# Optimization experiments

Hardware: AMD Instinct MI355X
Metric: run time of the kernel (lower is better)

## Reference

```python
import jax, jax.numpy as jnp
import numpy as np

N_NODES = 100000
N_EDGES = 1600000
D = 64


def _leaky(x, slope=0.2):
    return jnp.where(x >= 0, x, slope * x)


def setup_inputs() -> dict:
    key = jax.random.key(0)
    ks = jax.random.split(key, 13)
    x = jax.random.normal(ks[0], (N_NODES, D), dtype=jnp.float32)
    edge_index = jax.random.randint(ks[1], (2, N_EDGES), 0, N_NODES, dtype=jnp.int64)
    e_hat = jax.random.normal(ks[2], (N_EDGES, D), dtype=jnp.float32)
    s = 1.0 / np.sqrt(D)
    def lin(kw, kb):
        W = jax.random.uniform(kw, (D, D), dtype=jnp.float32, minval=-s, maxval=s)
        b = jax.random.uniform(kb, (D,), dtype=jnp.float32, minval=-s, maxval=s)
        return W, b
    U_w, U_b = lin(ks[3], ks[4])
    V_w, V_b = lin(ks[5], ks[6])
    A_w, A_b = lin(ks[7], ks[8])
    B_w, B_b = lin(ks[9], ks[10])
    C_w, C_b = lin(ks[11], ks[12])
    return {"x": x, "e_hat": e_hat, "edge_index": edge_index,
            "U_w": U_w, "U_b": U_b, "V_w": V_w, "V_b": V_b,
            "A_w": A_w, "A_b": A_b, "B_w": B_w, "B_b": B_b,
            "C_w": C_w, "C_b": C_b}


def reference(x, e_hat, edge_index, U_w, U_b, V_w, V_b, A_w, A_b, B_w, B_b, C_w, C_b):
    n = x.shape[0]
    src = edge_index[0]  # [E]
    dst = edge_index[1]  # [E]

    x_i = x[src]  # [E, D] (pre-update x, as in original)
    x_j = x[dst]  # [E, D]

    # scatter_softmax of e_hat over segments keyed by src, per feature column
    m = jax.ops.segment_max(e_hat, src, num_segments=n)        # [N, D]
    ex = jnp.exp(e_hat - m[src])                               # [E, D]
    denom = jax.ops.segment_sum(ex, src, num_segments=n)      # [N, D]
    e = ex / denom[src]                                        # [E, D]

    # gated aggregation: scatter_add(V(x_j) * e)
    y = (x_j @ V_w.T + V_b) * e                                # [E, D]
    y = jax.ops.segment_sum(y, src, num_segments=n)            # [N, D]

    x_new = x + _leaky(x @ U_w.T + U_b + y)
    e_new = e_hat + _leaky(x_i @ A_w.T + A_b + x_j @ B_w.T + B_b + e_hat @ C_w.T + C_b)
    return x_new, e_new
```

## Files before the change

### kernel.cpp

```cpp
#include <hip/hip_runtime.h>
#include <math.h>
#include <stdint.h>

typedef __attribute__((ext_vector_type(8))) short bf16x8;
typedef __attribute__((ext_vector_type(4))) float f32x4;

static __device__ __forceinline__ float leaky(float v) {
    return v >= 0.f ? v : 0.2f * v;
}

static __device__ __forceinline__ short f2bf(float f) {
    uint32_t u = __float_as_uint(f);
    u = (u + 0x7FFFu + ((u >> 16) & 1u)) >> 16;
    return (short)u;
}

static __device__ __forceinline__ float b2f(unsigned short us) {
    return __uint_as_float(((uint32_t)us) << 16);
}

static __device__ __forceinline__ bf16x8 pack8(float4 a, float4 b) {
    bf16x8 r;
    r[0] = f2bf(a.x); r[1] = f2bf(a.y); r[2] = f2bf(a.z); r[3] = f2bf(a.w);
    r[4] = f2bf(b.x); r[5] = f2bf(b.y); r[6] = f2bf(b.z); r[7] = f2bf(b.w);
    return r;
}

static __device__ __forceinline__ void split2(int bid, int na, int nb,
                                              bool& second, int& idx) {
    int nm = na < nb ? na : nb;
    if (bid < 2 * nm) { idx = bid >> 1; second = (bid & 1) != 0; }
    else { int r = bid - 2 * nm; second = nb > na; idx = nm + r; }
}

static __device__ __forceinline__ void load_wfrags_f32(const float* __restrict__ W,
                                                       int lo, int hi, bf16x8 wf[4][2]) {
#pragma unroll
    for (int ct = 0; ct < 4; ++ct)
#pragma unroll
        for (int s = 0; s < 2; ++s) {
            const float* cp = W + (size_t)(ct * 16 + lo) * 64 + s * 32 + hi * 8;
            wf[ct][s] = pack8(*(const float4*)cp, *(const float4*)(cp + 4));
        }
}

static __device__ __forceinline__ void load_wfrags(const unsigned short* __restrict__ Wb,
                                                   int lo, int hi, bf16x8 wf[4][2]) {
#pragma unroll
    for (int ct = 0; ct < 4; ++ct)
#pragma unroll
        for (int s = 0; s < 2; ++s)
            wf[ct][s] = *(const bf16x8*)(Wb + (size_t)(ct * 16 + lo) * 64 + s * 32 + hi * 8);
}

__global__ __launch_bounds__(256) void pre_fused(
        const float* __restrict__ x,
        const float* __restrict__ Uw, const float* __restrict__ Ub,
        const float* __restrict__ Vw, const float* __restrict__ Vb,
        const float* __restrict__ Aw, const float* __restrict__ Ab,
        const float* __restrict__ Bw, const float* __restrict__ Bb,
        const float* __restrict__ Cw, unsigned short* __restrict__ Cbf,
        float* __restrict__ Ux, unsigned short* __restrict__ Vxb,
        unsigned short* __restrict__ Axb, unsigned short* __restrict__ Bxb, int n,
        const int* __restrict__ src, int* __restrict__ deg, int e,
        int gemmBlocks, int histBlocks)
{
    int t = threadIdx.x;
    int bid = blockIdx.x;

    if (bid >= gemmBlocks + histBlocks) {
        int i = (bid - gemmBlocks - histBlocks) * 256 + t;
        Cbf[i] = (unsigned short)f2bf(Cw[i]);
        return;
    }

    bool isHist; int half;
    split2(bid, gemmBlocks, histBlocks, isHist, half);

    if (isHist) {
        int i0 = half * 1024 + t * 4;
        if (i0 + 3 < e) {
            int4 s4 = *(const int4*)(src + i0);
            atomicAdd(&deg[s4.x], 1); atomicAdd(&deg[s4.y], 1);
            atomicAdd(&deg[s4.z], 1); atomicAdd(&deg[s4.w], 1);
        } else {
#pragma unroll
            for (int k = 0; k < 4; ++k) { int i = i0 + k; if (i < e) atomicAdd(&deg[src[i]], 1); }
        }
        return;
    }

    int w = t >> 6, l = t & 63;
    int lo = l & 15, hi = l >> 4;
    long base = (long)half * 64;

    const float* Wp = (w == 0) ? Uw : (w == 1) ? Vw : (w == 2) ? Aw : Bw;
    const float* bp = (w == 0) ? Ub : (w == 1) ? Vb : (w == 2) ? Ab : Bb;

    bf16x8 wf[4][2];
    load_wfrags_f32(Wp, lo, hi, wf);

#pragma unroll
    for (int st = 0; st < 4; ++st) {
        long nd = base + st * 16 + lo;
        long ndc = nd < n ? nd : (long)n - 1;
        bf16x8 eb[2];
#pragma unroll
        for (int s = 0; s < 2; ++s) {
            const float* p = x + ndc * 64 + s * 32 + hi * 8;
            eb[s] = pack8(*(const float4*)p, *(const float4*)(p + 4));
        }
        f32x4 acc[4];
#pragma unroll
        for (int ct = 0; ct < 4; ++ct) {
            acc[ct] = (f32x4){0.f, 0.f, 0.f, 0.f};
            acc[ct] = __builtin_amdgcn_mfma_f32_16x16x32_bf16(wf[ct][0], eb[0], acc[ct], 0, 0, 0);
            acc[ct] = __builtin_amdgcn_mfma_f32_16x16x32_bf16(wf[ct][1], eb[1], acc[ct], 0, 0, 0);
        }
        if (nd < n) {
#pragma unroll
            for (int ct = 0; ct < 4; ++ct) {
                int c0 = ct * 16 + hi * 4;
                float4 bb = *(const float4*)(bp + c0);
                float o0 = acc[ct][0] + bb.x;
                float o1 = acc[ct][1] + bb.y;
                float o2 = acc[ct][2] + bb.z;
                float o3 = acc[ct][3] + bb.w;
                if (w == 0) {
                    *(float4*)(Ux + nd * 64 + c0) = make_float4(o0, o1, o2, o3);
                } else {
                    unsigned short* op = (w == 1) ? Vxb : (w == 2) ? Axb : Bxb;
                    ushort4 u = make_ushort4((unsigned short)f2bf(o0),
                                             (unsigned short)f2bf(o1),
                                             (unsigned short)f2bf(o2),
                                             (unsigned short)f2bf(o3));
                    *(ushort4*)(op + nd * 64 + c0) = u;
                }
            }
        }
    }
}

__global__ void scan_part(const int* __restrict__ deg, int* __restrict__ bsum, int n)
{
    int t = threadIdx.x;
    int i0 = blockIdx.x * 1024 + t * 4;
    int s = 0;
    if (i0 + 3 < n) {
        int4 d = *(const int4*)(deg + i0);
        s = d.x + d.y + d.z + d.w;
    } else {
#pragma unroll
        for (int k = 0; k < 4; ++k) { int i = i0 + k; if (i < n) s += deg[i]; }
    }
#pragma unroll
    for (int o = 1; o < 64; o <<= 1) s += __shfl_xor(s, o, 64);
    __shared__ int ws[4];
    if ((t & 63) == 0) ws[t >> 6] = s;
    __syncthreads();
    if (t == 0) bsum[blockIdx.x] = ws[0] + ws[1] + ws[2] + ws[3];
}

__global__ void scan_mid(int* __restrict__ bsum, int* __restrict__ rs, int nb, int n)
{
    __shared__ int tmp[128];
    int t = threadIdx.x;
    tmp[t] = (t < nb) ? bsum[t] : 0;
    __syncthreads();
    if (t == 0) {
        int run = 0;
        for (int i = 0; i < nb; ++i) { int v = tmp[i]; tmp[i] = run; run += v; }
        rs[n] = run;
    }
    __syncthreads();
    if (t < nb) bsum[t] = tmp[t];
}

__global__ void scan_out(const int* __restrict__ deg, const int* __restrict__ bsum,
                         int* __restrict__ rs, int* __restrict__ cursor, int n)
{
    int t = threadIdx.x;
    int i0 = blockIdx.x * 1024 + t * 4;
    int d[4]; int s = 0;
#pragma unroll
    for (int k = 0; k < 4; ++k) { int i = i0 + k; d[k] = (i < n) ? deg[i] : 0; s += d[k]; }
    int incl = s;
#pragma unroll
    for (int o = 1; o < 64; o <<= 1) {
        int u = __shfl_up(incl, o, 64);
        if ((t & 63) >= o) incl += u;
    }
    __shared__ int ws[4];
    if ((t & 63) == 63) ws[t >> 6] = incl;
    __syncthreads();
    int wofs = 0;
    for (int wv = 0; wv < (t >> 6); ++wv) wofs += ws[wv];
    int run = bsum[blockIdx.x] + wofs + incl - s;
#pragma unroll
    for (int k = 0; k < 4; ++k) {
        int i = i0 + k;
        if (i < n) { rs[i] = run; cursor[i] = run; run += d[k]; }
    }
}

__global__ void fill_kernel(const int* __restrict__ src, const int* __restrict__ dst,
                            int* __restrict__ cursor, int2* __restrict__ csr_ed, int e)
{
    int i = blockIdx.x * blockDim.x + threadIdx.x;
    if (i < e) {
        int s = src[i];
        int p = atomicAdd(&cursor[s], 1);
        csr_ed[p] = make_int2(i, dst[i]);
    }
}

__global__ __launch_bounds__(256) void fused_tail(
        const float* __restrict__ x, const float* __restrict__ ehat,
        const int* __restrict__ rs, const int2* __restrict__ csr_ed,
        const float* __restrict__ Ux, const unsigned short* __restrict__ Vxb,
        float* __restrict__ xnew, int n,
        const int* __restrict__ src, const int* __restrict__ dst,
        const unsigned short* __restrict__ Axb, const unsigned short* __restrict__ Bxb,
        const unsigned short* __restrict__ Cbf, const float* __restrict__ Cb,
        float* __restrict__ enew, int e, int nodeBlocks, int edgeBlocks)
{
    __shared__ __align__(16) float sacc[4][16][68];
    int t = threadIdx.x;
    bool isEdge; int half;
    split2(blockIdx.x, nodeBlocks, edgeBlocks, isEdge, half);

    if (!isEdge) {
        int lane = t & 63;
        int w = t >> 6;
#pragma unroll 1
        for (int q = 0; q < 4; ++q) {
            int wid = half * 16 + w * 4 + q;
            if (wid >= n) break;
            int beg = rs[wid];
            int end = rs[wid + 1];
            int o = wid * 64 + lane;
            float xo = x[o], uxo = Ux[o];
            float s = 0.f, y = 0.f;

            for (int pb = beg; pb < end; pb += 16) {
                int cnt = end - pb; cnt = cnt > 16 ? 16 : cnt;
                int2 ed[16];
#pragma unroll
                for (int u = 0; u < 16; ++u) ed[u] = csr_ed[pb + (u < cnt ? u : 0)];
                float v[16], vv[16];
#pragma unroll
                for (int u = 0; u < 16; ++u) {
                    v[u]  = ehat[(size_t)ed[u].x * 64 + lane];
                    vv[u] = b2f(Vxb[(size_t)ed[u].y * 64 + lane]);
                }
                asm volatile("" :: "v"(v[0]), "v"(v[1]), "v"(v[2]), "v"(v[3]),
                                   "v"(v[4]), "v"(v[5]), "v"(v[6]), "v"(v[7]),
                                   "v"(v[8]), "v"(v[9]), "v"(v[10]), "v"(v[11]),
                                   "v"(v[12]), "v"(v[13]), "v"(v[14]), "v"(v[15]));
                asm volatile("" :: "v"(vv[0]), "v"(vv[1]), "v"(vv[2]), "v"(vv[3]),
                                   "v"(vv[4]), "v"(vv[5]), "v"(vv[6]), "v"(vv[7]),
                                   "v"(vv[8]), "v"(vv[9]), "v"(vv[10]), "v"(vv[11]),
                                   "v"(vv[12]), "v"(vv[13]), "v"(vv[14]), "v"(vv[15]));
                float pw[8], py[8];
#pragma unroll
                for (int u = 0; u < 8; ++u) {
                    float ew = (u < cnt) ? __expf(v[u]) : 0.f;
                    pw[u] = ew;
                    py[u] = ew * vv[u];
                }
#pragma unroll
                for (int u = 8; u < 16; ++u) {
                    float ew = (u < cnt) ? __expf(v[u]) : 0.f;
                    pw[u - 8] += ew;
                    py[u - 8] += ew * vv[u];
                }
#pragma unroll
                for (int k = 0; k < 4; ++k) { pw[k] += pw[k + 4]; py[k] += py[k + 4]; }
                s += (pw[0] + pw[1]) + (pw[2] + pw[3]);
                y += (py[0] + py[1]) + (py[2] + py[3]);
            }
            float agg = (s > 0.f) ? y / s : 0.f;
            xnew[o] = xo + leaky(uxo + agg);
        }

    } else {
        int w = t >> 6, l = t & 63;
        int lo = l & 15, hi = l >> 4;

        bf16x8 wf[4][2];
        load_wfrags(Cbf, lo, hi, wf);
        float4 cb0[2], cb1[2];
#pragma unroll
        for (int s = 0; s < 2; ++s) {
            cb0[s] = *(const float4*)(Cb + s * 32 + hi * 8);
            cb1[s] = *(const float4*)(Cb + s * 32 + hi * 8 + 4);
        }

#pragma unroll 1
        for (int tt = 0; tt < 4; ++tt) {
            long base = (long)half * 256 + w * 64 + tt * 16;
            long rowA = base + lo;
            long rac = rowA < e ? rowA : (long)e - 1;

            int sn = src[rac], dn = dst[rac];

            float4 ra[2][2];
            bf16x8 a[2];
#pragma unroll
            for (int s = 0; s < 2; ++s) {
                const float* p = ehat + rac * 64 + s * 32 + hi * 8;
                ra[s][0] = *(const float4*)p;
                ra[s][1] = *(const float4*)(p + 4);
                a[s] = pack8(ra[s][0], ra[s][1]);
            }

            f32x4 acc[4];
#pragma unroll
            for (int ct = 0; ct < 4; ++ct) {
                acc[ct] = (f32x4){0.f, 0.f, 0.f, 0.f};
                acc[ct] = __builtin_amdgcn_mfma_f32_16x16x32_bf16(a[0], wf[ct][0], acc[ct], 0, 0, 0);
                acc[ct] = __builtin_amdgcn_mfma_f32_16x16x32_bf16(a[1], wf[ct][1], acc[ct], 0, 0, 0);
            }

#pragma unroll
            for (int ct = 0; ct < 4; ++ct)
#pragma unroll
                for (int i = 0; i < 4; ++i)
                    sacc[w][hi * 4 + i][ct * 16 + lo] = acc[ct][i];
            __builtin_amdgcn_wave_barrier();

            const unsigned short* apb = Axb + (size_t)sn * 64;
            const unsigned short* bpb = Bxb + (size_t)dn * 64;
            if (rowA < e) {
#pragma unroll
                for (int s = 0; s < 2; ++s) {
                    int c0 = s * 32 + hi * 8;
                    float4 ac0 = *(const float4*)&sacc[w][lo][c0];
                    float4 ac1 = *(const float4*)&sacc[w][lo][c0 + 4];
                    bf16x8 av8 = *(const bf16x8*)(apb + c0);
                    bf16x8 bv8 = *(const bf16x8*)(bpb + c0);
                    float4 o0, o1;
                    o0.x = ra[s][0].x + leaky(ac0.x + b2f((unsigned short)av8[0]) + b2f((unsigned short)bv8[0]) + cb0[s].x);
                    o0.y = ra[s][0].y + leaky(ac0.y + b2f((unsigned short)av8[1]) + b2f((unsigned short)bv8[1]) + cb0[s].y);
                    o0.z = ra[s][0].z + leaky(ac0.z + b2f((unsigned short)av8[2]) + b2f((unsigned short)bv8[2]) + cb0[s].z);
                    o0.w = ra[s][0].w + leaky(ac0.w + b2f((unsigned short)av8[3]) + b2f((unsigned short)bv8[3]) + cb0[s].w);
                    o1.x = ra[s][1].x + leaky(ac1.x + b2f((unsigned short)av8[4]) + b2f((unsigned short)bv8[4]) + cb1[s].x);
                    o1.y = ra[s][1].y + leaky(ac1.y + b2f((unsigned short)av8[5]) + b2f((unsigned short)bv8[5]) + cb1[s].y);
                    o1.z = ra[s][1].z + leaky(ac1.z + b2f((unsigned short)av8[6]) + b2f((unsigned short)bv8[6]) + cb1[s].z);
                    o1.w = ra[s][1].w + leaky(ac1.w + b2f((unsigned short)av8[7]) + b2f((unsigned short)bv8[7]) + cb1[s].w);
                    *(float4*)(enew + rowA * 64 + c0)     = o0;
                    *(float4*)(enew + rowA * 64 + c0 + 4) = o1;
                }
            }
        }
    }
}

extern "C" void kernel_launch(void* const* d_in, const int* in_sizes, int n_in,
                              void* d_out, int out_size, void* d_ws, size_t ws_size,
                              hipStream_t stream)
{
    const float* x    = (const float*)d_in[0];
    const float* ehat = (const float*)d_in[1];
    const int*   ei   = (const int*)d_in[2];
    const float* Uw = (const float*)d_in[3];
    const float* Ub = (const float*)d_in[4];
    const float* Vw = (const float*)d_in[5];
    const float* Vb = (const float*)d_in[6];
    const float* Aw = (const float*)d_in[7];
    const float* Ab = (const float*)d_in[8];
    const float* Bw = (const float*)d_in[9];
    const float* Bb = (const float*)d_in[10];
    const float* Cw = (const float*)d_in[11];
    const float* Cb = (const float*)d_in[12];

    int n = in_sizes[0] / 64;
    int e = in_sizes[1] / 64;
    const int* src = ei;
    const int* dst = ei + e;

    auto align = [](size_t v) { return (v + 255) & ~(size_t)255; };
    char* w = (char*)d_ws;
    int*  deg    = (int*)w;  w += align((size_t)n * 4);
    int*  cursor = (int*)w;  w += align((size_t)n * 4);
    int*  rs     = (int*)w;  w += align((size_t)(n + 1) * 4);
    int*  bsum   = (int*)w;  w += align(512);
    int2* csr_ed = (int2*)w; w += align((size_t)e * 8);
    float* Ux    = (float*)w; w += align((size_t)n * 64 * 4);
    unsigned short* Vxb = (unsigned short*)w; w += align((size_t)n * 64 * 2);
    unsigned short* Axb = (unsigned short*)w; w += align((size_t)n * 64 * 2);
    unsigned short* Bxb = (unsigned short*)w; w += align((size_t)n * 64 * 2);
    unsigned short* Cbf = (unsigned short*)w; w += align((size_t)4096 * 2);

    float* xnew = (float*)d_out;
    float* enew = xnew + (size_t)n * 64;

    hipMemsetAsync(deg, 0, (size_t)n * 4, stream);

    int gemmBlocks = (n + 63) / 64;
    int histBlocks = (e + 1023) / 1024;
    pre_fused<<<gemmBlocks + histBlocks + 16, 256, 0, stream>>>(
        x, Uw, Ub, Vw, Vb, Aw, Ab, Bw, Bb, Cw, Cbf, Ux, Vxb, Axb, Bxb, n,
        src, deg, e, gemmBlocks, histBlocks);

    int nbp = (n + 1023) / 1024;
    scan_part<<<nbp, 256, 0, stream>>>(deg, bsum, n);
    scan_mid<<<1, 128, 0, stream>>>(bsum, rs, nbp, n);
    scan_out<<<nbp, 256, 0, stream>>>(deg, bsum, rs, cursor, n);
    fill_kernel<<<(e + 255) / 256, 256, 0, stream>>>(src, dst, cursor, csr_ed, e);

    int nodeBlocks = (n + 15) / 16;
    int edgeBlocks = (e + 255) / 256;
    fused_tail<<<nodeBlocks + edgeBlocks, 256, 0, stream>>>(
        x, ehat, rs, csr_ed, Ux, Vxb, xnew, n,
        src, dst, Axb, Bxb, Cbf, Cb, enew, e, nodeBlocks, edgeBlocks);
}
```

Baseline: 621.4 us.

## Co-schedule edge update with CSR fill, run node aggregation separately

The edge-update MFMA work moves out of the final fused kernel and into the CSR fill kernel, so block-split dispatch runs the atomic fill and the edge output in the same launch. Node aggregation becomes its own kernel that runs after the CSR is complete. The aim is to hide the latency-bound atomic scatter behind the bandwidth-heavy edge GEMM epilogue. In exchange, fill blocks now compete with edge blocks for resources, and the node kernel no longer overlaps with edge work.

```diff
diff --git a/kernel.cpp b/kernel.cpp
--- a/kernel.cpp
+++ b/kernel.cpp
@@ -203,156 +203,158 @@
     }
 }
 
-__global__ void fill_kernel(const int* __restrict__ src, const int* __restrict__ dst,
-                            int* __restrict__ cursor, int2* __restrict__ csr_ed, int e)
-{
-    int i = blockIdx.x * blockDim.x + threadIdx.x;
-    if (i < e) {
-        int s = src[i];
-        int p = atomicAdd(&cursor[s], 1);
-        csr_ed[p] = make_int2(i, dst[i]);
-    }
-}
-
-__global__ __launch_bounds__(256) void fused_tail(
+__global__ __launch_bounds__(256) void fill_edge(
+        const int* __restrict__ src, const int* __restrict__ dst,
+        int* __restrict__ cursor, int2* __restrict__ csr_ed,
+        const float* __restrict__ ehat,
+        const unsigned short* __restrict__ Axb, const unsigned short* __restrict__ Bxb,
+        const unsigned short* __restrict__ Cbf, const float* __restrict__ Cb,
+        float* __restrict__ enew, int e, int fillBlocks, int edgeBlocks)
+{
+    __shared__ __align__(16) float sacc[4][16][68];
+    int t = threadIdx.x;
+    bool isEdge; int half;
+    split2(blockIdx.x, fillBlocks, edgeBlocks, isEdge, half);
+
+    if (!isEdge) {
+        int i = half * 256 + t;
+        if (i < e) {
+            int s = src[i];
+            int p = atomicAdd(&cursor[s], 1);
+            csr_ed[p] = make_int2(i, dst[i]);
+        }
+        return;
+    }
+
+    int w = t >> 6, l = t & 63;
+    int lo = l & 15, hi = l >> 4;
+
+    bf16x8 wf[4][2];
+    load_wfrags(Cbf, lo, hi, wf);
+    float4 cb0[2], cb1[2];
+#pragma unroll
+    for (int s = 0; s < 2; ++s) {
+        cb0[s] = *(const float4*)(Cb + s * 32 + hi * 8);
+        cb1[s] = *(const float4*)(Cb + s * 32 + hi * 8 + 4);
+    }
+
+#pragma unroll 1
+    for (int tt = 0; tt < 4; ++tt) {
+        long base = (long)half * 256 + w * 64 + tt * 16;
+        long rowA = base + lo;
+        long rac = rowA < e ? rowA : (long)e - 1;
+
+        int sn = src[rac], dn = dst[rac];
+
+        float4 ra[2][2];
+        bf16x8 a[2];
+#pragma unroll
+        for (int s = 0; s < 2; ++s) {
+            const float* p = ehat + rac * 64 + s * 32 + hi * 8;
+            ra[s][0] = *(const float4*)p;
+            ra[s][1] = *(const float4*)(p + 4);
+            a[s] = pack8(ra[s][0], ra[s][1]);
+        }
+
+        f32x4 acc[4];
+#pragma unroll
+        for (int ct = 0; ct < 4; ++ct) {
+            acc[ct] = (f32x4){0.f, 0.f, 0.f, 0.f};
+            acc[ct] = __builtin_amdgcn_mfma_f32_16x16x32_bf16(a[0], wf[ct][0], acc[ct], 0, 0, 0);
+            acc[ct] = __builtin_amdgcn_mfma_f32_16x16x32_bf16(a[1], wf[ct][1], acc[ct], 0, 0, 0);
+        }
+
+#pragma unroll
+        for (int ct = 0; ct < 4; ++ct)
+#pragma unroll
+            for (int i = 0; i < 4; ++i)
+                sacc[w][hi * 4 + i][ct * 16 + lo] = acc[ct][i];
+        __builtin_amdgcn_wave_barrier();
+
+        const unsigned short* apb = Axb + (size_t)sn * 64;
+        const unsigned short* bpb = Bxb + (size_t)dn * 64;
+        if (rowA < e) {
+#pragma unroll
+            for (int s = 0; s < 2; ++s) {
+                int c0 = s * 32 + hi * 8;
+                float4 ac0 = *(const float4*)&sacc[w][lo][c0];
+                float4 ac1 = *(const float4*)&sacc[w][lo][c0 + 4];
+                bf16x8 av8 = *(const bf16x8*)(apb + c0);
+                bf16x8 bv8 = *(const bf16x8*)(bpb + c0);
+                float4 o0, o1;
+                o0.x = ra[s][0].x + leaky(ac0.x + b2f((unsigned short)av8[0]) + b2f((unsigned short)bv8[0]) + cb0[s].x);
+                o0.y = ra[s][0].y + leaky(ac0.y + b2f((unsigned short)av8[1]) + b2f((unsigned short)bv8[1]) + cb0[s].y);
+                o0.z = ra[s][0].z + leaky(ac0.z + b2f((unsigned short)av8[2]) + b2f((unsigned short)bv8[2]) + cb0[s].z);
+                o0.w = ra[s][0].w + leaky(ac0.w + b2f((unsigned short)av8[3]) + b2f((unsigned short)bv8[3]) + cb0[s].w);
+                o1.x = ra[s][1].x + leaky(ac1.x + b2f((unsigned short)av8[4]) + b2f((unsigned short)bv8[4]) + cb1[s].x);
+                o1.y = ra[s][1].y + leaky(ac1.y + b2f((unsigned short)av8[5]) + b2f((unsigned short)bv8[5]) + cb1[s].y);
+                o1.z = ra[s][1].z + leaky(ac1.z + b2f((unsigned short)av8[6]) + b2f((unsigned short)bv8[6]) + cb1[s].z);
+                o1.w = ra[s][1].w + leaky(ac1.w + b2f((unsigned short)av8[7]) + b2f((unsigned short)bv8[7]) + cb1[s].w);
+                *(float4*)(enew + rowA * 64 + c0)     = o0;
+                *(float4*)(enew + rowA * 64 + c0 + 4) = o1;
+            }
+        }
+    }
+}
+
+__global__ __launch_bounds__(256) void node_agg(
         const float* __restrict__ x, const float* __restrict__ ehat,
         const int* __restrict__ rs, const int2* __restrict__ csr_ed,
         const float* __restrict__ Ux, const unsigned short* __restrict__ Vxb,
-        float* __restrict__ xnew, int n,
-        const int* __restrict__ src, const int* __restrict__ dst,
-        const unsigned short* __restrict__ Axb, const unsigned short* __restrict__ Bxb,
-        const unsigned short* __restrict__ Cbf, const float* __restrict__ Cb,
-        float* __restrict__ enew, int e, int nodeBlocks, int edgeBlocks)
-{
-    __shared__ __align__(16) float sacc[4][16][68];
-    int t = threadIdx.x;
-    bool isEdge; int half;
-    split2(blockIdx.x, nodeBlocks, edgeBlocks, isEdge, half);
-
-    if (!isEdge) {
-        int lane = t & 63;
-        int w = t >> 6;
+        float* __restrict__ xnew, int n)
+{
+    int t = threadIdx.x;
+    int lane = t & 63;
+    int w = t >> 6;
 #pragma unroll 1
-        for (int q = 0; q < 4; ++q) {
-            int wid = half * 16 + w * 4 + q;
-            if (wid >= n) break;
-            int beg = rs[wid];
-            int end = rs[wid + 1];
-            int o = wid * 64 + lane;
-            float xo = x[o], uxo = Ux[o];
-            float s = 0.f, y = 0.f;
-
-            for (int pb = beg; pb < end; pb += 16) {
-                int cnt = end - pb; cnt = cnt > 16 ? 16 : cnt;
-                int2 ed[16];
-#pragma unroll
-                for (int u = 0; u < 16; ++u) ed[u] = csr_ed[pb + (u < cnt ? u : 0)];
-                float v[16], vv[16];
-#pragma unroll
-                for (int u = 0; u < 16; ++u) {
-                    v[u]  = ehat[(size_t)ed[u].x * 64 + lane];
-                    vv[u] = b2f(Vxb[(size_t)ed[u].y * 64 + lane]);
-                }
-                asm volatile("" :: "v"(v[0]), "v"(v[1]), "v"(v[2]), "v"(v[3]),
-                                   "v"(v[4]), "v"(v[5]), "v"(v[6]), "v"(v[7]),
-                                   "v"(v[8]), "v"(v[9]), "v"(v[10]), "v"(v[11]),
-                                   "v"(v[12]), "v"(v[13]), "v"(v[14]), "v"(v[15]));
-                asm volatile("" :: "v"(vv[0]), "v"(vv[1]), "v"(vv[2]), "v"(vv[3]),
-                                   "v"(vv[4]), "v"(vv[5]), "v"(vv[6]), "v"(vv[7]),
-                                   "v"(vv[8]), "v"(vv[9]), "v"(vv[10]), "v"(vv[11]),
-                                   "v"(vv[12]), "v"(vv[13]), "v"(vv[14]), "v"(vv[15]));
-                float pw[8], py[8];
-#pragma unroll
-                for (int u = 0; u < 8; ++u) {
-                    float ew = (u < cnt) ? __expf(v[u]) : 0.f;
-                    pw[u] = ew;
-                    py[u] = ew * vv[u];
-                }
-#pragma unroll
-                for (int u = 8; u < 16; ++u) {
-                    float ew = (u < cnt) ? __expf(v[u]) : 0.f;
-                    pw[u - 8] += ew;
-                    py[u - 8] += ew * vv[u];
-                }
-#pragma unroll
-                for (int k = 0; k < 4; ++k) { pw[k] += pw[k + 4]; py[k] += py[k + 4]; }
-                s += (pw[0] + pw[1]) + (pw[2] + pw[3]);
-                y += (py[0] + py[1]) + (py[2] + py[3]);
+    for (int q = 0; q < 4; ++q) {
+        int wid = blockIdx.x * 16 + w * 4 + q;
+        if (wid >= n) break;
+        int beg = rs[wid];
+        int end = rs[wid + 1];
+        int o = wid * 64 + lane;
+        float xo = x[o], uxo = Ux[o];
+        float s = 0.f, y = 0.f;
+
+        for (int pb = beg; pb < end; pb += 16) {
+            int cnt = end - pb; cnt = cnt > 16 ? 16 : cnt;
+            int2 ed[16];
+#pragma unroll
+            for (int u = 0; u < 16; ++u) ed[u] = csr_ed[pb + (u < cnt ? u : 0)];
+            float v[16], vv[16];
+#pragma unroll
+            for (int u = 0; u < 16; ++u) {
+                v[u]  = ehat[(size_t)ed[u].x * 64 + lane];
+                vv[u] = b2f(Vxb[(size_t)ed[u].y * 64 + lane]);
             }
-            float agg = (s > 0.f) ? y / s : 0.f;
-            xnew[o] = xo + leaky(uxo + agg);
-        }
-
-    } else {
-        int w = t >> 6, l = t & 63;
-        int lo = l & 15, hi = l >> 4;
-
-        bf16x8 wf[4][2];
-        load_wfrags(Cbf, lo, hi, wf);
-        float4 cb0[2], cb1[2];
-#pragma unroll
-        for (int s = 0; s < 2; ++s) {
-            cb0[s] = *(const float4*)(Cb + s * 32 + hi * 8);
-            cb1[s] = *(const float4*)(Cb + s * 32 + hi * 8 + 4);
-        }
-
-#pragma unroll 1
-        for (int tt = 0; tt < 4; ++tt) {
-            long base = (long)half * 256 + w * 64 + tt * 16;
-            long rowA = base + lo;
-            long rac = rowA < e ? rowA : (long)e - 1;
-
-            int sn = src[rac], dn = dst[rac];
-
-            float4 ra[2][2];
-            bf16x8 a[2];
-#pragma unroll
-            for (int s = 0; s < 2; ++s) {
-                const float* p = ehat + rac * 64 + s * 32 + hi * 8;
-                ra[s][0] = *(const float4*)p;
-                ra[s][1] = *(const float4*)(p + 4);
-                a[s] = pack8(ra[s][0], ra[s][1]);
+            asm volatile("" :: "v"(v[0]), "v"(v[1]), "v"(v[2]), "v"(v[3]),
+                               "v"(v[4]), "v"(v[5]), "v"(v[6]), "v"(v[7]),
+                               "v"(v[8]), "v"(v[9]), "v"(v[10]), "v"(v[11]),
+                               "v"(v[12]), "v"(v[13]), "v"(v[14]), "v"(v[15]));
+            asm volatile("" :: "v"(vv[0]), "v"(vv[1]), "v"(vv[2]), "v"(vv[3]),
+                               "v"(vv[4]), "v"(vv[5]), "v"(vv[6]), "v"(vv[7]),
+                               "v"(vv[8]), "v"(vv[9]), "v"(vv[10]), "v"(vv[11]),
+                               "v"(vv[12]), "v"(vv[13]), "v"(vv[14]), "v"(vv[15]));
+            float pw[8], py[8];
+#pragma unroll
+            for (int u = 0; u < 8; ++u) {
+                float ew = (u < cnt) ? __expf(v[u]) : 0.f;
+                pw[u] = ew;
+                py[u] = ew * vv[u];
             }
-
-            f32x4 acc[4];
-#pragma unroll
-            for (int ct = 0; ct < 4; ++ct) {
-                acc[ct] = (f32x4){0.f, 0.f, 0.f, 0.f};
-                acc[ct] = __builtin_amdgcn_mfma_f32_16x16x32_bf16(a[0], wf[ct][0], acc[ct], 0, 0, 0);
-                acc[ct] = __builtin_amdgcn_mfma_f32_16x16x32_bf16(a[1], wf[ct][1], acc[ct], 0, 0, 0);
+#pragma unroll
+            for (int u = 8; u < 16; ++u) {
+                float ew = (u < cnt) ? __expf(v[u]) : 0.f;
+                pw[u - 8] += ew;
+                py[u - 8] += ew * vv[u];
             }
-
-#pragma unroll
-            for (int ct = 0; ct < 4; ++ct)
-#pragma unroll
-                for (int i = 0; i < 4; ++i)
-                    sacc[w][hi * 4 + i][ct * 16 + lo] = acc[ct][i];
-            __builtin_amdgcn_wave_barrier();
-
-            const unsigned short* apb = Axb + (size_t)sn * 64;
-            const unsigned short* bpb = Bxb + (size_t)dn * 64;
-            if (rowA < e) {
-#pragma unroll
-                for (int s = 0; s < 2; ++s) {
-                    int c0 = s * 32 + hi * 8;
-                    float4 ac0 = *(const float4*)&sacc[w][lo][c0];
-                    float4 ac1 = *(const float4*)&sacc[w][lo][c0 + 4];
-                    bf16x8 av8 = *(const bf16x8*)(apb + c0);
-                    bf16x8 bv8 = *(const bf16x8*)(bpb + c0);
-                    float4 o0, o1;
-                    o0.x = ra[s][0].x + leaky(ac0.x + b2f((unsigned short)av8[0]) + b2f((unsigned short)bv8[0]) + cb0[s].x);
-                    o0.y = ra[s][0].y + leaky(ac0.y + b2f((unsigned short)av8[1]) + b2f((unsigned short)bv8[1]) + cb0[s].y);
-                    o0.z = ra[s][0].z + leaky(ac0.z + b2f((unsigned short)av8[2]) + b2f((unsigned short)bv8[2]) + cb0[s].z);
-                    o0.w = ra[s][0].w + leaky(ac0.w + b2f((unsigned short)av8[3]) + b2f((unsigned short)bv8[3]) + cb0[s].w);
-                    o1.x = ra[s][1].x + leaky(ac1.x + b2f((unsigned short)av8[4]) + b2f((unsigned short)bv8[4]) + cb1[s].x);
-                    o1.y = ra[s][1].y + leaky(ac1.y + b2f((unsigned short)av8[5]) + b2f((unsigned short)bv8[5]) + cb1[s].y);
-                    o1.z = ra[s][1].z + leaky(ac1.z + b2f((unsigned short)av8[6]) + b2f((unsigned short)bv8[6]) + cb1[s].z);
-                    o1.w = ra[s][1].w + leaky(ac1.w + b2f((unsigned short)av8[7]) + b2f((unsigned short)bv8[7]) + cb1[s].w);
-                    *(float4*)(enew + rowA * 64 + c0)     = o0;
-                    *(float4*)(enew + rowA * 64 + c0 + 4) = o1;
-                }
-            }
-        }
+#pragma unroll
+            for (int k = 0; k < 4; ++k) { pw[k] += pw[k + 4]; py[k] += py[k + 4]; }
+            s += (pw[0] + pw[1]) + (pw[2] + pw[3]);
+            y += (py[0] + py[1]) + (py[2] + py[3]);
+        }
+        float agg = (s > 0.f) ? y / s : 0.f;
+        xnew[o] = xo + leaky(uxo + agg);
     }
 }
 
@@ -407,11 +409,14 @@
     scan_part<<<nbp, 256, 0, stream>>>(deg, bsum, n);
     scan_mid<<<1, 128, 0, stream>>>(bsum, rs, nbp, n);
     scan_out<<<nbp, 256, 0, stream>>>(deg, bsum, rs, cursor, n);
-    fill_kernel<<<(e + 255) / 256, 256, 0, stream>>>(src, dst, cursor, csr_ed, e);
+
+    int fillBlocks = (e + 255) / 256;
+    int edgeBlocks = (e + 255) / 256;
+    fill_edge<<<fillBlocks + edgeBlocks, 256, 0, stream>>>(
+        src, dst, cursor, csr_ed, ehat, Axb, Bxb, Cbf, Cb, enew, e,
+        fillBlocks, edgeBlocks);
 
     int nodeBlocks = (n + 15) / 16;
-    int edgeBlocks = (e + 255) / 256;
-    fused_tail<<<nodeBlocks + edgeBlocks, 256, 0, stream>>>(
-        x, ehat, rs, csr_ed, Ux, Vxb, xnew, n,
-        src, dst, Axb, Bxb, Cbf, Cb, enew, e, nodeBlocks, edgeBlocks);
-}
+    node_agg<<<nodeBlocks, 256, 0, stream>>>(
+        x, ehat, rs, csr_ed, Ux, Vxb, xnew, n);
+}
```

New measurement: 685.1 us. +10.3%, slower.
